# Optimization experiments

Measured on AMD Instinct MI355X. Metric: run time of the kernel, lower is better.

The kernel has to match this reference:

```python
import jax, jax.numpy as jnp
from jax import lax
import numpy as np

STRIDES = [4, 8, 16, 32, 64]
SIZES = [32, 64, 128, 256, 512]
RATIOS = [0.5, 1.0, 2.0]
PRE_NMS = 1000   # test-mode pre_nms_topk per level
POST_NMS = 1000  # test-mode post_nms_topk
NMS_THRESH = 0.7
NEG = -1e9
SCALE_CLAMP = float(np.log(1000.0 / 16.0))


def _anchor_bases(size):
    # one size, 3 aspect ratios (h/w); detectron2-style bases centered at 0
    area = float(size) * float(size)
    rows = []
    for ar in RATIOS:
        w = np.sqrt(area / ar)
        h = ar * w
        rows.append([-w / 2.0, -h / 2.0, w / 2.0, h / 2.0])
    return jnp.asarray(np.array(rows, dtype=np.float32))  # [3,4]


def _level_anchors(H, W, stride, bases):
    sx = jnp.arange(W, dtype=jnp.float32) * stride
    sy = jnp.arange(H, dtype=jnp.float32) * stride
    yy, xx = jnp.meshgrid(sy, sx, indexing='ij')
    shifts = jnp.stack([xx, yy, xx, yy], axis=-1).reshape(-1, 1, 4)  # [H*W,1,4]
    return (shifts + bases[None, :, :]).reshape(-1, 4)  # [H*W*3,4]


def _conv(x, w, b, pad):
    y = lax.conv_general_dilated(x, w, (1, 1), [(pad, pad), (pad, pad)],
                                 dimension_numbers=('NCHW', 'OIHW', 'NCHW'))
    return y + b[None, :, None, None]


def _decode(anchors, deltas):
    # anchors [R,4], deltas [B,R,4] -> boxes [B,R,4] (x1,y1,x2,y2)
    w = anchors[:, 2] - anchors[:, 0]
    h = anchors[:, 3] - anchors[:, 1]
    cx = anchors[:, 0] + 0.5 * w
    cy = anchors[:, 1] + 0.5 * h
    dx, dy = deltas[..., 0], deltas[..., 1]
    dw = jnp.minimum(deltas[..., 2], SCALE_CLAMP)
    dh = jnp.minimum(deltas[..., 3], SCALE_CLAMP)
    px = dx * w + cx
    py = dy * h + cy
    pw = jnp.exp(dw) * w
    ph = jnp.exp(dh) * h
    return jnp.stack([px - 0.5 * pw, py - 0.5 * ph, px + 0.5 * pw, py + 0.5 * ph], axis=-1)


def _pairwise_iou(b):
    x1 = jnp.maximum(b[:, None, 0], b[None, :, 0])
    y1 = jnp.maximum(b[:, None, 1], b[None, :, 1])
    x2 = jnp.minimum(b[:, None, 2], b[None, :, 2])
    y2 = jnp.minimum(b[:, None, 3], b[None, :, 3])
    inter = jnp.clip(x2 - x1, 0.0) * jnp.clip(y2 - y1, 0.0)
    area = (b[:, 2] - b[:, 0]) * (b[:, 3] - b[:, 1])
    return inter / (area[:, None] + area[None, :] - inter + 1e-9)


def _nms_single(boxes, scores, valid, lvls, img):
    # greedy batched NMS: level offsets keep levels from suppressing each other
    order = jnp.argsort(-scores)
    b = boxes[order]
    s = scores[order]
    v = valid[order]
    lv = lvls[order].astype(boxes.dtype)
    bo = b + lv[:, None] * (img + 1.0)
    iou = lax.stop_gradient(_pairwise_iou(bo))  # selection is non-differentiable
    T = b.shape[0]
    idxs = jnp.arange(T)

    def step(keep, i):
        supp = (iou[i] > NMS_THRESH) & (idxs > i) & keep[i]
        return keep & ~supp, None

    keep, _ = lax.scan(step, v, jnp.arange(T))
    final = jnp.where(keep, s, NEG)
    topv, topi = lax.top_k(final, POST_NMS)
    return b[topi], topv


def _rpn_forward(feats, w_inter, b_inter, w_logits, b_logits, w_reg, b_reg, image_size):
    img = float(image_size)
    cand_boxes, cand_scores, lvl_ids = [], [], []
    for l, (x, stride, size) in enumerate(zip(feats, STRIDES, SIZES)):
        B, _, H, W = x.shape
        inter = jax.nn.relu(_conv(x, w_inter, b_inter, 1))
        logit = _conv(inter, w_logits, b_logits, 0)        # [B,3,H,W]
        reg = _conv(inter, w_reg, b_reg, 0)                # [B,12,H,W]
        scores = logit.transpose(0, 2, 3, 1).reshape(B, -1)              # [B,H*W*3]
        deltas = reg.reshape(B, 3, 4, H, W).transpose(0, 3, 4, 1, 2).reshape(B, -1, 4)
        anchors = _level_anchors(H, W, stride, _anchor_bases(size))
        boxes = _decode(anchors, deltas)                                  # [B,R,4]
        k = min(PRE_NMS, scores.shape[1])
        topv, topi = lax.top_k(scores, k)
        cand_boxes.append(jnp.take_along_axis(boxes, topi[..., None], axis=1))
        cand_scores.append(topv)
        lvl_ids.append(jnp.full((k,), l, dtype=jnp.int32))
    boxes = jnp.concatenate(cand_boxes, axis=1)   # [B,T,4]
    scores = jnp.concatenate(cand_scores, axis=1) # [B,T]
    lvls = jnp.concatenate(lvl_ids, axis=0)       # [T]
    boxes = jnp.clip(boxes, 0.0, img)
    valid = (boxes[..., 2] > boxes[..., 0]) & (boxes[..., 3] > boxes[..., 1])
    kb, ks = jax.vmap(lambda b, s, v: _nms_single(b, s, v, lvls, img))(boxes, scores, valid)
    return jnp.concatenate([kb, ks[..., None]], axis=-1)  # [B,POST_NMS,5]


def setup_inputs() -> dict:
    key = jax.random.key(0)
    ks = jax.random.split(key, 16)
    C = 256
    inp = {
        'feat_p2': jax.random.normal(ks[0], (2, C, 256, 256), jnp.float32),
        'feat_p3': jax.random.normal(ks[1], (2, C, 128, 128), jnp.float32),
        'feat_p4': jax.random.normal(ks[2], (2, C, 64, 64), jnp.float32),
        'feat_p5': jax.random.normal(ks[3], (2, C, 32, 32), jnp.float32),
        'feat_p6': jax.random.normal(ks[4], (2, C, 16, 16), jnp.float32),
        'w_inter': jax.random.normal(ks[5], (C, C, 3, 3), jnp.float32) * 0.01,
        'b_inter': jnp.zeros((C,), jnp.float32),
        'w_logits': jax.random.normal(ks[6], (3, C, 1, 1), jnp.float32) * 0.01,
        'b_logits': jnp.zeros((3,), jnp.float32),
        'w_reg': jax.random.normal(ks[7], (12, C, 1, 1), jnp.float32) * 0.01,
        'b_reg': jnp.zeros((12,), jnp.float32),
        'image_size': 1024,
    }
    return inp


def reference(feat_p2, feat_p3, feat_p4, feat_p5, feat_p6,
              w_inter, b_inter, w_logits, b_logits, w_reg, b_reg, image_size):
    feats = [feat_p2, feat_p3, feat_p4, feat_p5, feat_p6]
    return _rpn_forward(feats, w_inter, b_inter, w_logits, b_logits, w_reg, b_reg, image_size)
```

## Files before the change

kernel.cpp:

```cpp
#include <hip/hip_runtime.h>
#include <cmath>

typedef unsigned int u32;
typedef unsigned long long u64;

#define TCAND 4768
#define RTOT  261888
#define NW    75
#define NROWS 4800
#define NEGV  -1e9f

__device__ __forceinline__ u32 fkey(float s){
  u32 u = __float_as_uint(s);
  return u ^ ((u >> 31) ? 0xFFFFFFFFu : 0x80000000u);
}

__device__ __forceinline__ void gload_lds16(const float* g, float* l){
  __builtin_amdgcn_global_load_lds((const __attribute__((address_space(1))) void*)g,
                                   (__attribute__((address_space(3))) void*)l, 16, 0, 0);
}
__device__ __forceinline__ void gload_lds4(const float* g, float* l){
  __builtin_amdgcn_global_load_lds((const __attribute__((address_space(1))) void*)g,
                                   (__attribute__((address_space(3))) void*)l, 4, 0, 0);
}

__device__ void bitonic_desc(u64* a, int N, int t, int nt){
  for (int len = 2; len <= N; len <<= 1){
    for (int inc = len >> 1; inc > 0; inc >>= 1){
      __syncthreads();
      for (int idx = t; idx < (N >> 1); idx += nt){
        int i = 2*idx - (idx & (inc - 1));
        int j = i + inc;
        u64 x = a[i], y = a[j];
        bool descR = ((i & len) == 0);
        bool sw = descR ? (x < y) : (x > y);
        if (sw){ a[i] = y; a[j] = x; }
      }
    }
  }
  __syncthreads();
}

__global__ void wtrans(const float* __restrict__ w, float* __restrict__ w_r2,
                       float* __restrict__ zbuf){
  if (blockIdx.x == 0 && threadIdx.x < 16) zbuf[threadIdx.x] = 0.f;
  int idx = blockIdx.x * 256 + threadIdx.x;
  if (idx >= 589824) return;
  int ic = idx / 2304;
  int f  = idx - ic * 2304;
  int tap = f >> 8;
  int oc  = f & 255;
  w_r2[idx] = w[oc * 2304 + ic * 9 + tap];
}

template<int H, int STRIDEV, int ASIZE, int FOFF>
__device__ __forceinline__ void conv_level(
    int rel, const float* __restrict__ feat, const float* __restrict__ w_r2,
    const float* __restrict__ zbuf,
    const float* __restrict__ b_inter, const float* __restrict__ w_logits,
    const float* __restrict__ b_logits, const float* __restrict__ w_reg,
    const float* __restrict__ b_reg, const int* __restrict__ imgp,
    float* __restrict__ score_base, float* __restrict__ box_base,
    float* lds_w, float* lds_x, float* sbuf)
{
  constexpr int W = H;
  constexpr int TX = H / 8;
  constexpr int TILES = TX * TX;
  const int t = threadIdx.x;
  const int img = rel / TILES;
  const int tile = rel - img * TILES;
  const int x0 = (tile % TX) << 3;
  const int y0 = (tile / TX) << 3;
  const int lane = t & 63;
  const int ocg = lane;
  const int r = t >> 6;
  const int q = r;

  const size_t fb = (size_t)img * 256 * H * W;
  const size_t plane = (size_t)H * W;

  const float* xsrc = zbuf;
  size_t xstep = 0;
  if (q == 1 || q == 2){
    int cell = (q - 1) * 64 + lane;
    int xr = cell / 12, xc = cell - xr * 12;
    int gy = y0 + xr - 1, gx = x0 + xc - 1;
    bool ok = (cell < 120) && (xc < 10) && gy >= 0 && gy < H && gx >= 0 && gx < W;
    if (ok){ xsrc = feat + fb + (size_t)gy * W + gx; xstep = plane; }
  }

  const int c0 = 2 * q, c1 = 2 * q + 1;
  const int cex = (q == 0) ? 16 : ((q == 3) ? 17 : -1);

  float acc[32];
  #pragma unroll
  for (int j = 0; j < 32; j++) acc[j] = 0.f;

  #define STAGE(g_, sb) do { \
    const float* wg_ = w_r2 + (size_t)(g_) * 4608; \
    float* wl_ = lds_w + (sb) * 4608; \
    gload_lds16(wg_ + c0 * 256 + lane * 4, wl_ + c0 * 256); \
    gload_lds16(wg_ + c1 * 256 + lane * 4, wl_ + c1 * 256); \
    if (cex >= 0) gload_lds16(wg_ + cex * 256 + lane * 4, wl_ + cex * 256); \
    if (q == 1 || q == 2){ \
      gload_lds4(xsrc + (size_t)(2 * (g_)) * xstep, \
                 lds_x + (sb) * 256 + (q - 1) * 64); \
      gload_lds4(xsrc + (size_t)(2 * (g_) + 1) * xstep, \
                 lds_x + (sb) * 256 + 128 + (q - 1) * 64); \
    } \
  } while (0)

  STAGE(0, 0);

  int cur = 0;
  #pragma unroll 1
  for (int g = 0; g < 128; ++g){
    __builtin_amdgcn_s_barrier();
    __builtin_amdgcn_sched_barrier(0);
    if (g < 127){
      STAGE(g + 1, cur ^ 1);
    }
    __builtin_amdgcn_sched_barrier(0);
    if (g < 127){
      if (q == 1 || q == 2)      asm volatile("s_waitcnt vmcnt(4)" ::: "memory");
      else if (q == 0 || q == 3) asm volatile("s_waitcnt vmcnt(3)" ::: "memory");
      else                       asm volatile("s_waitcnt vmcnt(2)" ::: "memory");
    } else {
      asm volatile("s_waitcnt vmcnt(0)" ::: "memory");
    }
    __builtin_amdgcn_sched_barrier(0);
    __builtin_amdgcn_s_barrier();
    __builtin_amdgcn_sched_barrier(0);

    const float* wbuf = lds_w + cur * 4608;
    const float* xbuf = lds_x + cur * 256;
    #pragma unroll 1
    for (int icl = 0; icl < 2; icl++){
      const float* wsub = wbuf + icl * 2304;
      const float* xsub = xbuf + icl * 128;
      #pragma unroll
      for (int ky = 0; ky < 3; ky++){
        float xrow[10];
        {
          const float* xp = xsub + (r + ky) * 12;
          *(float4*)&xrow[0] = *(const float4*)xp;
          *(float4*)&xrow[4] = *(const float4*)(xp + 4);
          *(float2*)&xrow[8] = *(const float2*)(xp + 8);
        }
        #pragma unroll
        for (int kx = 0; kx < 3; kx++){
          const int tap = ky * 3 + kx;
          float wk[4];
          *(float4*)&wk[0] = *(const float4*)(wsub + tap * 256 + ocg * 4);
          #pragma unroll
          for (int k = 0; k < 4; k++){
            #pragma unroll
            for (int c = 0; c < 8; c++)
              acc[k * 8 + c] = __builtin_fmaf(wk[k], xrow[c + kx], acc[k * 8 + c]);
          }
        }
      }
    }
    cur ^= 1;
  }
  #undef STAGE

  {
    float bb[4];
    *(float4*)&bb[0] = *(const float4*)(b_inter + ocg * 4);
    #pragma unroll
    for (int k = 0; k < 4; k++)
      #pragma unroll
      for (int c = 0; c < 8; c++)
        acc[k * 8 + c] = fmaxf(acc[k * 8 + c] + bb[k], 0.f);
  }

  const int grp = ocg & 60;
  #pragma unroll 1
  for (int o = 0; o < 15; o++){
    const float* whp = (o < 3) ? (w_logits + o * 256) : (w_reg + (o - 3) * 256);
    float wh4[4];
    *(float4*)&wh4[0] = *(const float4*)(whp + ocg * 4);
    float fin[8];
    #pragma unroll
    for (int c = 0; c < 8; c++){
      float t1 = 0.f;
      #pragma unroll
      for (int k = 0; k < 4; k++) t1 = __builtin_fmaf(wh4[k], acc[k * 8 + c], t1);
      float b1 = __shfl(t1, grp);
      float t2 = b1;
      #pragma unroll
      for (int k = 0; k < 4; k++) t2 = __builtin_fmaf(wh4[k], acc[k * 8 + c], t2);
      float b2 = __shfl(t2, grp + 1);
      float t3 = b2;
      #pragma unroll
      for (int k = 0; k < 4; k++) t3 = __builtin_fmaf(wh4[k], acc[k * 8 + c], t3);
      float b3 = __shfl(t3, grp + 2);
      float t4 = b3;
      #pragma unroll
      for (int k = 0; k < 4; k++) t4 = __builtin_fmaf(wh4[k], acc[k * 8 + c], t4);
      float v = t4 + __shfl_xor(t4, 4);
      v = v + __shfl_xor(v, 8);
      v = v + __shfl_xor(v, 16);
      v = v + __shfl_xor(v, 32);
      fin[c] = v;
    }
    if (ocg == 3){
      #pragma unroll
      for (int c = 0; c < 8; c++) sbuf[(r * 8 + c) * 16 + o] = fin[c];
    }
  }
  __syncthreads();

  if (t < 192){
    int a = t >> 6; int px = t & 63;
    int rr = px >> 3, cc = px & 7;
    int y = y0 + rr, x = x0 + cc;
    float img_f = (float)(*imgp);
    float sc = sbuf[px * 16 + a] + b_logits[a];
    float d0 = sbuf[px * 16 + 3 + a * 4 + 0] + b_reg[a * 4 + 0];
    float d1 = sbuf[px * 16 + 3 + a * 4 + 1] + b_reg[a * 4 + 1];
    float d2 = sbuf[px * 16 + 3 + a * 4 + 2] + b_reg[a * 4 + 2];
    float d3 = sbuf[px * 16 + 3 + a * 4 + 3] + b_reg[a * 4 + 3];
    double ar = (a == 0) ? 0.5 : ((a == 1) ? 1.0 : 2.0);
    double area_d = (double)ASIZE * (double)ASIZE;
    double wd = sqrt(area_d / ar);
    double hd = ar * wd;
    float bx1 = (float)(-wd * 0.5), by1 = (float)(-hd * 0.5);
    float bx2 = (float)( wd * 0.5), by2 = (float)( hd * 0.5);
    float sx = (float)(x * STRIDEV), sy = (float)(y * STRIDEV);
    float ax1 = sx + bx1, ay1 = sy + by1, ax2 = sx + bx2, ay2 = sy + by2;
    float aw = __fsub_rn(ax2, ax1), ah = __fsub_rn(ay2, ay1);
    float acx = __fadd_rn(ax1, __fmul_rn(0.5f, aw));
    float acy = __fadd_rn(ay1, __fmul_rn(0.5f, ah));
    const float CLAMP = (float)4.135166556742356;
    float dwv = fminf(d2, CLAMP), dhv = fminf(d3, CLAMP);
    float pcx = __fadd_rn(__fmul_rn(d0, aw), acx);
    float pcy = __fadd_rn(__fmul_rn(d1, ah), acy);
    float pw = __fmul_rn((float)exp((double)dwv), aw);
    float ph = __fmul_rn((float)exp((double)dhv), ah);
    float hx = __fmul_rn(0.5f, pw), hy = __fmul_rn(0.5f, ph);
    float X1 = __fsub_rn(pcx, hx), Y1 = __fsub_rn(pcy, hy);
    float X2 = __fadd_rn(pcx, hx), Y2 = __fadd_rn(pcy, hy);
    X1 = fminf(fmaxf(X1, 0.f), img_f); Y1 = fminf(fmaxf(Y1, 0.f), img_f);
    X2 = fminf(fmaxf(X2, 0.f), img_f); Y2 = fminf(fmaxf(Y2, 0.f), img_f);
    int gi = (y * W + x) * 3 + a;
    size_t oidx = (size_t)img * RTOT + FOFF + gi;
    score_base[oidx] = sc;
    ((float4*)box_base)[oidx] = make_float4(X1, Y1, X2, Y2);
  }
}

__global__ __launch_bounds__(512, 4) void conv_all(
    const float* __restrict__ f2, const float* __restrict__ f3,
    const float* __restrict__ f4, const float* __restrict__ f5,
    const float* __restrict__ f6, const float* __restrict__ w_r2,
    const float* __restrict__ zbuf,
    const float* __restrict__ b_inter, const float* __restrict__ w_logits,
    const float* __restrict__ b_logits, const float* __restrict__ w_reg,
    const float* __restrict__ b_reg, const int* __restrict__ imgp,
    float* __restrict__ score_base, float* __restrict__ box_base)
{
  __shared__ float lds_w[2 * 4608];
  __shared__ float lds_x[2 * 256];
  __shared__ float sbuf[64 * 16];
  const int bid = blockIdx.x;
  if (bid < 2048)
    conv_level<256, 4, 32, 0>(bid, f2, w_r2, zbuf, b_inter, w_logits, b_logits, w_reg,
                              b_reg, imgp, score_base, box_base, lds_w, lds_x, sbuf);
  else if (bid < 2560)
    conv_level<128, 8, 64, 196608>(bid - 2048, f3, w_r2, zbuf, b_inter, w_logits, b_logits,
                                   w_reg, b_reg, imgp, score_base, box_base, lds_w, lds_x, sbuf);
  else if (bid < 2688)
    conv_level<64, 16, 128, 245760>(bid - 2560, f4, w_r2, zbuf, b_inter, w_logits, b_logits,
                                    w_reg, b_reg, imgp, score_base, box_base, lds_w, lds_x, sbuf);
  else if (bid < 2720)
    conv_level<32, 32, 256, 258048>(bid - 2688, f5, w_r2, zbuf, b_inter, w_logits, b_logits,
                                    w_reg, b_reg, imgp, score_base, box_base, lds_w, lds_x, sbuf);
  else
    conv_level<16, 64, 512, 261120>(bid - 2720, f6, w_r2, zbuf, b_inter, w_logits, b_logits,
                                    w_reg, b_reg, imgp, score_base, box_base, lds_w, lds_x, sbuf);
}

__global__ __launch_bounds__(1024) void topk_lvl(
    const float* __restrict__ score_base, const float* __restrict__ box_base,
    float* __restrict__ cs, float* __restrict__ cb, int* __restrict__ clvl)
{
  const int lvl = blockIdx.x, b = blockIdx.y;
  const int Rtab[5] = {196608, 49152, 12288, 3072, 768};
  const int Ktab[5] = {1000, 1000, 1000, 1000, 768};
  const int Ftab[5] = {0, 196608, 245760, 258048, 261120};
  const int Ctab[5] = {0, 1000, 2000, 3000, 4000};
  const int R = Rtab[lvl], kk = Ktab[lvl], foff = Ftab[lvl], coff = Ctab[lvl];
  const float* sc = score_base + (size_t)b * RTOT + foff;
  const int t = threadIdx.x;
  __shared__ u32 hist[256];
  __shared__ u32 sh_prefix, sh_r;
  __shared__ u32 cgt, ceq;
  __shared__ u64 sel[1024];
  __shared__ u64 eqb[1024];
  if (t == 0){ sh_prefix = 0u; sh_r = (u32)kk; }
  __syncthreads();
  for (int pass = 0; pass < 4; ++pass){
    if (t < 256) hist[t] = 0u;
    __syncthreads();
    u32 prefix = sh_prefix;
    int shift = 24 - 8 * pass;
    u32 maskHi = (pass == 0) ? 0u : (0xFFFFFFFFu << (shift + 8));
    for (int i = t; i < R; i += 1024){
      u32 key = fkey(sc[i]);
      if ((key & maskHi) == prefix) atomicAdd(&hist[(key >> shift) & 255u], 1u);
    }
    __syncthreads();
    if (t == 0){
      u32 r = sh_r; u32 run = 0; int chosen = 255;
      for (int bv = 255; bv >= 0; --bv){
        u32 c = hist[bv];
        if (run + c >= r){ chosen = bv; break; }
        run += c;
      }
      sh_prefix = prefix | ((u32)chosen << shift);
      sh_r = r - run;
    }
    __syncthreads();
  }
  const u32 Tkey = sh_prefix; const u32 need_eq = sh_r;
  if (t == 0){ cgt = 0u; ceq = 0u; }
  __syncthreads();
  for (int i = t; i < R; i += 1024){
    u32 key = fkey(sc[i]);
    if (key > Tkey){
      u32 p = atomicAdd(&cgt, 1u);
      sel[p] = (((u64)key) << 32) | (u64)(0xFFFFFFFFu - (u32)i);
    } else if (key == Tkey){
      u32 e = atomicAdd(&ceq, 1u);
      if (e < 1024u) eqb[e] = (u64)(0xFFFFFFFFu - (u32)i);
    }
  }
  __syncthreads();
  u32 nGt = cgt; u32 nEq = ceq > 1024u ? 1024u : ceq;
  if ((u32)t >= nEq) eqb[t] = 0ull;
  __syncthreads();
  bitonic_desc(eqb, 1024, t, 1024);
  if ((u32)t < need_eq) sel[nGt + t] = (((u64)Tkey) << 32) | (eqb[t] & 0xFFFFFFFFull);
  if (t >= kk) sel[t] = 0ull;
  __syncthreads();
  bitonic_desc(sel, 1024, t, 1024);
  if (t < kk){
    u64 v = sel[t];
    u32 i = 0xFFFFFFFFu - (u32)(v & 0xFFFFFFFFull);
    int dst = b * TCAND + coff + t;
    cs[dst] = sc[i];
    ((float4*)cb)[dst] = ((const float4*)box_base)[(size_t)b * RTOT + foff + i];
    clvl[dst] = lvl;
  }
}

__global__ __launch_bounds__(1024) void gsort(
    const float* __restrict__ cs, const float* __restrict__ cb, const int* __restrict__ clvl,
    const int* __restrict__ imgp,
    float* __restrict__ s_score, float* __restrict__ s_box, float* __restrict__ obox,
    float* __restrict__ area, int* __restrict__ validarr)
{
  const int b = blockIdx.x, t = threadIdx.x;
  __shared__ u64 arr[8192];
  for (int i = t; i < 8192; i += 1024){
    u64 v = 0ull;
    if (i < TCAND){
      u32 key = fkey(cs[b * TCAND + i]);
      v = (((u64)key) << 32) | (u64)(0xFFFFFFFFu - (u32)i);
    }
    arr[i] = v;
  }
  __syncthreads();
  bitonic_desc(arr, 8192, t, 1024);
  const float img = (float)(*imgp);
  const float off1 = img + 1.0f;
  for (int s = t; s < TCAND; s += 1024){
    u32 ci = 0xFFFFFFFFu - (u32)(arr[s] & 0xFFFFFFFFull);
    int src = b * TCAND + (int)ci;
    int dst = b * TCAND + s;
    float scv = cs[src];
    float4 bx = ((const float4*)cb)[src];
    s_score[dst] = scv;
    ((float4*)s_box)[dst] = bx;
    float lv = (float)clvl[src];
    float tt = __fmul_rn(lv, off1);
    float o0 = __fadd_rn(bx.x, tt), o1 = __fadd_rn(bx.y, tt);
    float o2 = __fadd_rn(bx.z, tt), o3 = __fadd_rn(bx.w, tt);
    ((float4*)obox)[dst] = make_float4(o0, o1, o2, o3);
    area[dst] = __fmul_rn(__fsub_rn(o2, o0), __fsub_rn(o3, o1));
    validarr[dst] = (bx.z > bx.x && bx.w > bx.y) ? 1 : 0;
  }
}

__global__ void iou_mat(const float* __restrict__ obox, const float* __restrict__ area,
                        u64* __restrict__ supp)
{
  const int b = blockIdx.y;
  int wid = blockIdx.x * 256 + threadIdx.x;
  const int total = TCAND * NW;
  if (wid >= total) return;
  int i = wid / NW, w = wid - i * NW;
  float4 bi = ((const float4*)obox)[b * TCAND + i];
  float ai = area[b * TCAND + i];
  u64 bits = 0ull;
  int jbase = w << 6;
  for (int jj = 0; jj < 64; jj++){
    int j = jbase + jj;
    if (j >= TCAND) break;
    if (j <= i) continue;
    float4 bj = ((const float4*)obox)[b * TCAND + j];
    float xx1 = fmaxf(bi.x, bj.x), yy1 = fmaxf(bi.y, bj.y);
    float xx2 = fminf(bi.z, bj.z), yy2 = fminf(bi.w, bj.w);
    float iw = fmaxf(__fsub_rn(xx2, xx1), 0.f);
    float ih = fmaxf(__fsub_rn(yy2, yy1), 0.f);
    float inter = __fmul_rn(iw, ih);
    float uni = __fadd_rn(__fsub_rn(__fadd_rn(ai, area[b * TCAND + j]), inter), 1e-9f);
    float iou = inter / uni;
    if (iou > 0.7f) bits |= (1ull << jj);
  }
  supp[((size_t)b * NROWS + i) * NW + w] = bits;
}

__global__ __launch_bounds__(64) void nms_scan(const u64* __restrict__ supp,
                                               const int* __restrict__ validarr,
                                               u64* __restrict__ keep_out)
{
  const int b = blockIdx.x;
  const int lane = threadIdx.x;
  u64 rlo = 0ull, rhi = 0ull;
  for (int jj = 0; jj < 64; jj++){
    int i1 = (lane << 6) + jj;
    u64 bad1 = (i1 < TCAND) ? (validarr[b * TCAND + i1] ? 0ull : 1ull) : 1ull;
    rlo |= bad1 << jj;
    int i2 = ((lane + 64) << 6) + jj;
    u64 bad2 = (i2 < TCAND) ? (validarr[b * TCAND + i2] ? 0ull : 1ull) : 1ull;
    rhi |= bad2 << jj;
  }
  for (int c = 0; c < NW; c++){
    u64 rw = (c < 64) ? __shfl(rlo, c) : __shfl(rhi, c - 64);
    u64 diag = supp[((size_t)b * NROWS + (c << 6) + lane) * NW + c];
    for (int s = 0; s < 64; s++){
      if (!((rw >> s) & 1ull)) rw |= __shfl(diag, s);
    }
    if (c < 64){ if (lane == c) rlo = rw; }
    else       { if (lane == c - 64) rhi = rw; }
    u64 kept = ~rw;
    const u64* rowbase = supp + ((size_t)b * NROWS + (c << 6)) * NW;
    for (int s = 0; s < 64; s++){
      if ((kept >> s) & 1ull){
        rlo |= rowbase[(size_t)s * NW + lane];
        if (lane < 11) rhi |= rowbase[(size_t)s * NW + 64 + lane];
      }
    }
  }
  keep_out[b * 80 + lane] = ~rlo;
  if (lane < 11) keep_out[b * 80 + 64 + lane] = ~rhi;
}

__global__ __launch_bounds__(1024) void emit(const u64* __restrict__ keep_out,
                                             const float* __restrict__ s_score,
                                             const float* __restrict__ s_box,
                                             float* __restrict__ out)
{
  const int b = blockIdx.x, t = threadIdx.x;
  __shared__ int part[1024];
  int f[5]; int base = t * 5; int lsum = 0;
  #pragma unroll
  for (int q = 0; q < 5; q++){
    int s = base + q; int kp = 0;
    if (s < TCAND) kp = (int)((keep_out[b * 80 + (s >> 6)] >> (s & 63)) & 1ull);
    f[q] = kp; lsum += kp;
  }
  part[t] = lsum;
  __syncthreads();
  for (int d = 1; d < 1024; d <<= 1){
    int addv = 0;
    if (t >= d) addv = part[t - d];
    __syncthreads();
    part[t] += addv;
    __syncthreads();
  }
  int K = part[1023];
  int kcnt = part[t] - lsum;
  #pragma unroll
  for (int q = 0; q < 5; q++){
    int s = base + q;
    if (s < TCAND){
      int pos = f[q] ? kcnt : (K + (s - kcnt));
      if (pos < 1000){
        float4 bx = ((const float4*)s_box)[b * TCAND + s];
        float scv = f[q] ? s_score[b * TCAND + s] : NEGV;
        float* o = out + ((size_t)b * 1000 + pos) * 5;
        o[0] = bx.x; o[1] = bx.y; o[2] = bx.z; o[3] = bx.w; o[4] = scv;
      }
      kcnt += f[q];
    }
  }
}

extern "C" void kernel_launch(void* const* d_in, const int* in_sizes, int n_in,
                              void* d_out, int out_size, void* d_ws, size_t ws_size,
                              hipStream_t stream)
{
  (void)in_sizes; (void)n_in; (void)out_size; (void)ws_size;
  const float* f2 = (const float*)d_in[0];
  const float* f3 = (const float*)d_in[1];
  const float* f4 = (const float*)d_in[2];
  const float* f5 = (const float*)d_in[3];
  const float* f6 = (const float*)d_in[4];
  const float* w_inter  = (const float*)d_in[5];
  const float* b_inter  = (const float*)d_in[6];
  const float* w_logits = (const float*)d_in[7];
  const float* b_logits = (const float*)d_in[8];
  const float* w_reg    = (const float*)d_in[9];
  const float* b_reg    = (const float*)d_in[10];
  const int*   imgp     = (const int*)d_in[11];

  char* ws = (char*)d_ws;
  float* w_r2       = (float*)(ws + 0);
  float* score_base = (float*)(ws + 2359296);
  float* box_base   = (float*)(ws + 4454400);
  float* cs         = (float*)(ws + 12834816);
  float* cb         = (float*)(ws + 12872960);
  int*   clvl       = (int*)  (ws + 13025536);
  float* s_score    = (float*)(ws + 13063680);
  float* s_box      = (float*)(ws + 13101824);
  float* obox       = (float*)(ws + 13254400);
  float* area       = (float*)(ws + 13406976);
  int*   validarr   = (int*)  (ws + 13445120);
  u64*   supp       = (u64*)  (ws + 13483264);
  u64*   keep_out   = (u64*)  (ws + 19243264);
  float* zbuf       = (float*)(ws + 13483264);

  hipLaunchKernelGGL(wtrans, dim3((589824 + 255) / 256), dim3(256), 0, stream,
                     w_inter, w_r2, zbuf);

  hipLaunchKernelGGL(conv_all, dim3(2728), dim3(512), 0, stream,
                     f2, f3, f4, f5, f6, w_r2, zbuf, b_inter, w_logits, b_logits,
                     w_reg, b_reg, imgp, score_base, box_base);

  hipLaunchKernelGGL(topk_lvl, dim3(5, 2), dim3(1024), 0, stream,
                     score_base, box_base, cs, cb, clvl);
  hipLaunchKernelGGL(gsort, dim3(2), dim3(1024), 0, stream,
                     cs, cb, clvl, imgp, s_score, s_box, obox, area, validarr);
  hipLaunchKernelGGL(iou_mat, dim3((TCAND * NW + 255) / 256, 2), dim3(256), 0, stream,
                     obox, area, supp);
  hipLaunchKernelGGL(nms_scan, dim3(2), dim3(64), 0, stream, supp, validarr, keep_out);
  hipLaunchKernelGGL(emit, dim3(2), dim3(1024), 0, stream, keep_out, s_score, s_box,
                     (float*)d_out);
}
```

Measured before the change: 4.726 ms.

## Coalesce weight transpose, privatize radix histograms, remap IoU threads, batch NMS row loads

The weight transpose now reads coalesced and scatters its writes. The top-k radix select gives each wavefront its own LDS histogram and merges them afterwards, which cuts atomic contention. The IoU kernel swaps its thread mapping so consecutive threads take consecutive boxes i within one word column. This makes the bj loads uniform across the wave but leaves the supp writes strided. The NMS scan walks only the kept bits with ctz and issues four row loads at once for more memory-level parallelism.

```diff
diff --git a/kernel.cpp b/kernel.cpp
--- a/kernel.cpp
+++ b/kernel.cpp
@@ -46,11 +46,11 @@
   if (blockIdx.x == 0 && threadIdx.x < 16) zbuf[threadIdx.x] = 0.f;
   int idx = blockIdx.x * 256 + threadIdx.x;
   if (idx >= 589824) return;
-  int ic = idx / 2304;
-  int f  = idx - ic * 2304;
-  int tap = f >> 8;
-  int oc  = f & 255;
-  w_r2[idx] = w[oc * 2304 + ic * 9 + tap];
+  int oc = idx / 2304;
+  int r  = idx - oc * 2304;
+  int ic = r / 9;
+  int tap = r - ic * 9;
+  w_r2[ic * 2304 + tap * 256 + oc] = w[idx];
 }
 
 template<int H, int STRIDEV, int ASIZE, int FOFF>
@@ -294,6 +294,8 @@
   const int R = Rtab[lvl], kk = Ktab[lvl], foff = Ftab[lvl], coff = Ctab[lvl];
   const float* sc = score_base + (size_t)b * RTOT + foff;
   const int t = threadIdx.x;
+  const int wv = t >> 6;
+  __shared__ u32 histp[16 * 256];
   __shared__ u32 hist[256];
   __shared__ u32 sh_prefix, sh_r;
   __shared__ u32 cgt, ceq;
@@ -302,14 +304,21 @@
   if (t == 0){ sh_prefix = 0u; sh_r = (u32)kk; }
   __syncthreads();
   for (int pass = 0; pass < 4; ++pass){
-    if (t < 256) hist[t] = 0u;
+    for (int i = t; i < 4096; i += 1024) histp[i] = 0u;
     __syncthreads();
     u32 prefix = sh_prefix;
     int shift = 24 - 8 * pass;
     u32 maskHi = (pass == 0) ? 0u : (0xFFFFFFFFu << (shift + 8));
     for (int i = t; i < R; i += 1024){
       u32 key = fkey(sc[i]);
-      if ((key & maskHi) == prefix) atomicAdd(&hist[(key >> shift) & 255u], 1u);
+      if ((key & maskHi) == prefix) atomicAdd(&histp[wv * 256 + ((key >> shift) & 255u)], 1u);
+    }
+    __syncthreads();
+    if (t < 256){
+      u32 s = 0;
+      #pragma unroll
+      for (int w2 = 0; w2 < 16; w2++) s += histp[w2 * 256 + t];
+      hist[t] = s;
     }
     __syncthreads();
     if (t == 0){
@@ -399,9 +408,10 @@
 {
   const int b = blockIdx.y;
   int wid = blockIdx.x * 256 + threadIdx.x;
-  const int total = TCAND * NW;
+  const int total = NW * TCAND;
   if (wid >= total) return;
-  int i = wid / NW, w = wid - i * NW;
+  int w = wid / TCAND;
+  int i = wid - w * TCAND;
   float4 bi = ((const float4*)obox)[b * TCAND + i];
   float ai = area[b * TCAND + i];
   u64 bits = 0ull;
@@ -448,10 +458,24 @@
     else       { if (lane == c - 64) rhi = rw; }
     u64 kept = ~rw;
     const u64* rowbase = supp + ((size_t)b * NROWS + (c << 6)) * NW;
-    for (int s = 0; s < 64; s++){
-      if ((kept >> s) & 1ull){
-        rlo |= rowbase[(size_t)s * NW + lane];
-        if (lane < 11) rhi |= rowbase[(size_t)s * NW + 64 + lane];
+    u64 rem = kept;
+    while (rem){
+      int s0 = (int)__builtin_ctzll(rem); rem &= rem - 1;
+      int s1 = s0, s2 = s0, s3 = s0;
+      if (rem){ s1 = (int)__builtin_ctzll(rem); rem &= rem - 1; }
+      if (rem){ s2 = (int)__builtin_ctzll(rem); rem &= rem - 1; }
+      if (rem){ s3 = (int)__builtin_ctzll(rem); rem &= rem - 1; }
+      u64 a0 = rowbase[(size_t)s0 * NW + lane];
+      u64 a1 = rowbase[(size_t)s1 * NW + lane];
+      u64 a2 = rowbase[(size_t)s2 * NW + lane];
+      u64 a3 = rowbase[(size_t)s3 * NW + lane];
+      rlo |= (a0 | a1) | (a2 | a3);
+      if (lane < 11){
+        u64 h0 = rowbase[(size_t)s0 * NW + 64 + lane];
+        u64 h1 = rowbase[(size_t)s1 * NW + 64 + lane];
+        u64 h2 = rowbase[(size_t)s2 * NW + 64 + lane];
+        u64 h3 = rowbase[(size_t)s3 * NW + 64 + lane];
+        rhi |= (h0 | h1) | (h2 | h3);
       }
     }
   }
@@ -545,7 +569,7 @@
                      score_base, box_base, cs, cb, clvl);
   hipLaunchKernelGGL(gsort, dim3(2), dim3(1024), 0, stream,
                      cs, cb, clvl, imgp, s_score, s_box, obox, area, validarr);
-  hipLaunchKernelGGL(iou_mat, dim3((TCAND * NW + 255) / 256, 2), dim3(256), 0, stream,
+  hipLaunchKernelGGL(iou_mat, dim3((NW * TCAND + 255) / 256, 2), dim3(256), 0, stream,
                      obox, area, supp);
   hipLaunchKernelGGL(nms_scan, dim3(2), dim3(64), 0, stream, supp, validarr, keep_out);
   hipLaunchKernelGGL(emit, dim3(2), dim3(1024), 0, stream, keep_out, s_score, s_box,
```

Result: faster. 3.998 ms (-15.4%).
